# Optimization experiments

Measured on AMD Instinct MI355X. Metric: run time of the kernel, lower is better.

Reference implementation:

```python
import jax, jax.numpy as jnp
import numpy as np

SCALE = 4.0
GRID = 64
B, T, A, C = 4, 256, 3, 13
F = 5 + C  # x,y,z,r,conf,cls...


def setup_inputs() -> dict:
    key = jax.random.key(0)
    k1, k2, k3, k4, k5 = jax.random.split(key, 5)
    p = jax.random.normal(k1, (B, A, GRID, GRID, GRID, F), dtype=jnp.float32)
    xyz = jax.random.uniform(k2, (B, T, 3), minval=4.0, maxval=SCALE * GRID - 4.0)
    r = jax.random.uniform(k3, (B, T, 1), minval=6.0, maxval=20.0)
    conf = (jax.random.uniform(k4, (B, T, 1)) < 0.6).astype(jnp.float32)
    cls = jax.nn.one_hot(jax.random.randint(k5, (B, T), 0, C), C, dtype=jnp.float32)
    targets = jnp.concatenate([xyz, r, conf, cls], axis=-1)  # [B,T,18]
    anchor = jnp.array([[[8.0], [12.0], [16.0]]], dtype=jnp.float32)  # [1,A,1]
    return {"p": p, "targets": targets, "anchor": anchor}


def _bce(logits, t):
    # BCEWithLogitsLoss (pos_weight=1), elementwise
    return t * jax.nn.softplus(-logits) + (1.0 - t) * jax.nn.softplus(logits)


def _eiou(box1, box2, eps=1e-7):
    # boxes are (x,y,z,r): axis-aligned cubes of side r centered at xyz (3D EIoU)
    c1, r1 = box1[:, :3], box1[:, 3]
    c2, r2 = box2[:, :3], box2[:, 3]
    h1, h2 = r1[:, None] * 0.5, r2[:, None] * 0.5
    lo = jnp.maximum(c1 - h1, c2 - h2)
    hi = jnp.minimum(c1 + h1, c2 + h2)
    inter = jnp.prod(jnp.clip(hi - lo, 0.0), axis=-1)
    union = r1 ** 3 + r2 ** 3 - inter + eps
    iou = inter / union
    clo = jnp.minimum(c1 - h1, c2 - h2)
    chi = jnp.maximum(c1 + h1, c2 + h2)
    cdim = chi - clo  # enclosing box per-axis extent
    rho2 = jnp.sum((c1 - c2) ** 2, axis=-1)
    c2diag = jnp.sum(cdim ** 2, axis=-1) + eps
    size_pen = jnp.sum(((r1 - r2) ** 2)[:, None] / (cdim ** 2 + eps), axis=-1)
    return iou - rho2 / c2diag - size_pen


def reference(p, targets, anchor):
    Bs, An, K, J, I, Fd = p.shape
    Cn = Fd - 5
    g, gr = 0.5, 0.0
    Tn = targets.shape[1]
    n = Bs * Tn
    x = targets.reshape(n, Fd)
    b0 = jnp.repeat(jnp.arange(Bs), Tn)
    conf_m = x[:, 4] > 0.5
    anchor_norm = anchor[0] / SCALE  # [A,1]
    gxyzr = x[:, :4] / SCALE
    rn = gxyzr[:, 3]
    ratio = rn[None, :] / anchor_norm  # [A,n]
    aok = jnp.maximum(ratio, 1.0 / ratio) < 4.0
    gxyz = gxyzr[:, :3]
    gdim = jnp.array([K, J, I], dtype=p.dtype)  # gain[1:]
    gxyz_i = gdim - gxyz
    m1 = (gxyz % 1.0 < g) & (gxyz > 1.0)
    m2 = (gxyz_i % 1.0 < g) & (gxyz_i > 1.0)
    fm = jnp.stack([jnp.ones_like(m1[:, 0]), m1[:, 0], m1[:, 1], m1[:, 2], m2[:, 0], m2[:, 1], m2[:, 2]])  # [7,n]
    off = jnp.array([[0, 0, 0], [1, 0, 0], [0, 1, 0], [0, 0, 1], [-1, 0, 0], [0, -1, 0], [0, 0, -1]], dtype=p.dtype) * g
    valid = (conf_m[None, None, :] & aok[None, :, :] & fm[:, None, :]).reshape(-1)  # [7*A*n]
    bidx = jnp.broadcast_to(b0[None, None, :], (7, An, n)).reshape(-1)
    aidx = jnp.broadcast_to(jnp.arange(An)[None, :, None], (7, An, n)).reshape(-1)
    gxyz_c = jnp.broadcast_to(gxyz[None, None], (7, An, n, 3))
    off_c = jnp.broadcast_to(off[:, None, None, :], (7, An, n, 3))
    gijk_f = jnp.trunc(jax.lax.stop_gradient(gxyz_c - off_c))  # torch .long() truncates
    gijk = gijk_f.astype(jnp.int32).reshape(-1, 3)
    gi = jnp.clip(gijk[:, 0], 0, I - 1)
    gj = jnp.clip(gijk[:, 1], 0, J - 1)
    gk = jnp.clip(gijk[:, 2], 0, K - 1)
    tbox = jnp.concatenate([(gxyz_c - gijk_f).reshape(-1, 3), jnp.broadcast_to(rn[None, None, :], (7, An, n)).reshape(-1, 1)], axis=1)
    anchors = anchor_norm[aidx]  # [N,1]
    tcls = jnp.broadcast_to(x[None, None, :, 5:], (7, An, n, Cn)).reshape(-1, Cn)
    pred = p[bidx, aidx, gk, gj, gi]  # [N,F]
    pxyz = jax.nn.sigmoid(pred[:, :3]) * 2.0 - 0.5
    pr = (jax.nn.sigmoid(pred[:, 3:4]) * 2.0) ** 2 * anchors
    pbox = jnp.concatenate([pxyz, pr], axis=1)
    ei = _eiou(pbox, tbox)
    w = valid.astype(p.dtype)
    nv = jnp.maximum(jnp.sum(w), 1.0)
    loss_bbox = jnp.sum(w * (1.0 - ei)) / nv  # masked mean == torch mean over filtered rows
    iou_d = jax.lax.stop_gradient(jnp.clip(ei, 0.0))
    objv = (1.0 - gr) + gr * iou_d  # gr=0 -> 1.0
    tobj = jnp.zeros((Bs, An, K, J, I), dtype=p.dtype).at[bidx, aidx, gk, gj, gi].max(w * objv)
    loss_cls = jnp.sum(w[:, None] * _bce(pred[:, 5:], tcls)) / (nv * Cn)
    loss_obj = jnp.mean(_bce(p[..., 4], tobj))
    lb = loss_bbox * 1.0
    lo = loss_obj * 20.0
    lc = loss_cls * 10.0
    return ((lb + lo + lc) * Bs, lo, lc)
```

## Files before the change

### kernel.cpp

```cpp
#include <hip/hip_runtime.h>
#include <math.h>

#define NTGT   1024
#define NCAND  (21 * NTGT)
#define NCBLK  (NCAND / 256)
#define NCELL  (4 * 3 * 64 * 64 * 64)
#define BITW   (NCELL / 32)
#define NBLK   2048

__device__ __forceinline__ float softplusf(float x) {
    return fmaxf(x, 0.0f) + __logf(1.0f + __expf(-fabsf(x)));
}
__device__ __forceinline__ float sigmoidf(float x) {
    return 1.0f / (1.0f + __expf(-x));
}

__global__ __launch_bounds__(256) void fused_kernel(
    const float* __restrict__ p, const float* __restrict__ tg,
    const float* __restrict__ anchor, float* __restrict__ acc,
    unsigned int* __restrict__ bitmap)
{
    if (blockIdx.x < NCBLK) {
        int idx = blockIdx.x * 256 + threadIdx.x;
        float nv_v = 0.f, bb_v = 0.f, cl_v = 0.f, ob_v = 0.f;
        {
            int t  = idx & (NTGT - 1);
            int oa = idx >> 10;
            int a  = oa % 3;
            int o  = oa / 3;
            const float* x = tg + t * 18;
            float conf = x[4];
            float rn   = x[3] * 0.25f;
            float an   = anchor[a] * 0.25f;
            float ratio = rn / an;
            bool ok = (conf > 0.5f) && (fmaxf(ratio, 1.0f / ratio) < 4.0f);
            float gv[3] = { x[0] * 0.25f, x[1] * 0.25f, x[2] * 0.25f };
            float off[3] = { 0.f, 0.f, 0.f };
            if (o >= 1) {
                if (o <= 3) {
                    int c = o - 1;
                    float v = gv[c];
                    ok = ok && ((v - floorf(v)) < 0.5f) && (v > 1.0f);
                    off[c] = 0.5f;
                } else {
                    int c = o - 4;
                    float vi = 64.0f - gv[c];
                    ok = ok && ((vi - floorf(vi)) < 0.5f) && (vi > 1.0f);
                    off[c] = -0.5f;
                }
            }
            if (ok) {
                float tb[3]; int gq[3];
                #pragma unroll
                for (int c = 0; c < 3; c++) {
                    float f = truncf(gv[c] - off[c]);
                    tb[c] = gv[c] - f;
                    gq[c] = min(max((int)f, 0), 63);
                }
                int b0 = t >> 8;
                unsigned int cell =
                    ((((unsigned)(b0 * 3 + a) * 64u + (unsigned)gq[2]) * 64u
                      + (unsigned)gq[1]) * 64u) + (unsigned)gq[0];
                const float* pp = p + (size_t)cell * 18u;
                float pd[18];
                #pragma unroll
                for (int f = 0; f < 18; f++) pd[f] = pp[f];

                float c1[3];
                #pragma unroll
                for (int c = 0; c < 3; c++) c1[c] = sigmoidf(pd[c]) * 2.0f - 0.5f;
                float s4 = sigmoidf(pd[3]) * 2.0f;
                float r1 = s4 * s4 * an;
                float r2 = rn;

                float h1 = 0.5f * r1, h2 = 0.5f * r2;
                float inter = 1.f, rho2 = 0.f, c2d = 0.f, spen = 0.f;
                float dr2 = (r1 - r2) * (r1 - r2);
                #pragma unroll
                for (int c = 0; c < 3; c++) {
                    float lo1 = c1[c] - h1, hi1 = c1[c] + h1;
                    float lo2 = tb[c] - h2, hi2 = tb[c] + h2;
                    inter *= fmaxf(fminf(hi1, hi2) - fmaxf(lo1, lo2), 0.f);
                    float cd  = fmaxf(hi1, hi2) - fminf(lo1, lo2);
                    float cd2 = cd * cd;
                    float d   = c1[c] - tb[c];
                    rho2 += d * d;
                    c2d  += cd2;
                    spen += dr2 / (cd2 + 1e-7f);
                }
                float uni = r1 * r1 * r1 + r2 * r2 * r2 - inter + 1e-7f;
                float ei  = inter / uni - rho2 / (c2d + 1e-7f) - spen;

                nv_v = 1.0f;
                bb_v = 1.0f - ei;
                float cl = 0.f;
                #pragma unroll
                for (int c = 0; c < 13; c++) {
                    float l = pd[5 + c];
                    cl += softplusf(l) - x[5 + c] * l;
                }
                cl_v = cl;
                unsigned int old = atomicOr(&bitmap[cell >> 5], 1u << (cell & 31u));
                if (!(old & (1u << (cell & 31u)))) ob_v = pd[4];
            }
        }
        #pragma unroll
        for (int s = 32; s > 0; s >>= 1) {
            nv_v += __shfl_down(nv_v, s, 64);
            bb_v += __shfl_down(bb_v, s, 64);
            cl_v += __shfl_down(cl_v, s, 64);
            ob_v += __shfl_down(ob_v, s, 64);
        }
        if ((threadIdx.x & 63) == 0 && nv_v != 0.f) {
            atomicAdd(&acc[0], nv_v);
            atomicAdd(&acc[1], bb_v);
            atomicAdd(&acc[2], cl_v);
            atomicAdd(&acc[4], ob_v);
        }
    }

    float s = 0.f;
    {
        int i = blockIdx.x * 256 + threadIdx.x;
        #pragma unroll
        for (int it = 0; it < NCELL / (NBLK * 256); it++) {
            s += softplusf(p[(size_t)i * 18u + 4u]);
            i += NBLK * 256;
        }
    }
    #pragma unroll
    for (int sh = 32; sh > 0; sh >>= 1) s += __shfl_down(s, sh, 64);
    __shared__ float sm[4];
    int lane = threadIdx.x & 63, w = threadIdx.x >> 6;
    if (lane == 0) sm[w] = s;
    __syncthreads();
    if (threadIdx.x == 0) {
        atomicAdd(&acc[3], sm[0] + sm[1] + sm[2] + sm[3]);
    }
}

__global__ void final_kernel(const float* __restrict__ acc, float* __restrict__ out)
{
    float nv = fmaxf(acc[0], 1.0f);
    float lb = acc[1] / nv;
    float lc = acc[2] / (nv * 13.0f) * 10.0f;
    float lo = (acc[3] - acc[4]) * (20.0f / (float)NCELL);
    out[0] = (lb + lo + lc) * 4.0f;
    out[1] = lo;
    out[2] = lc;
}

extern "C" void kernel_launch(void* const* d_in, const int* in_sizes, int n_in,
                              void* d_out, int out_size, void* d_ws, size_t ws_size,
                              hipStream_t stream) {
    const float* p       = (const float*)d_in[0];
    const float* targets = (const float*)d_in[1];
    const float* anchor  = (const float*)d_in[2];
    float* out = (float*)d_out;

    float* acc = (float*)d_ws;
    unsigned int* bitmap = (unsigned int*)((char*)d_ws + 32);

    hipMemsetAsync(d_ws, 0, 32 + (size_t)BITW * 4, stream);

    fused_kernel<<<NBLK, 256, 0, stream>>>(p, targets, anchor, acc, bitmap);
    final_kernel<<<1, 1, 0, stream>>>(acc, out);
}
```

Baseline: 311.0 us.

## Fold final reduction into fused kernel via last-block counter

Removes the separate single-thread finalize launch. The last block to finish, detected with an atomic counter behind a threadfence, computes the three loss outputs itself. It also adds a min-blocks launch bound of 8 and reads prediction fields directly from global memory instead of staging all 18 into registers, aiming to cut register pressure and raise occupancy. The main risks are the atomic counter's ordering and possible repeated loads from pp.

```diff
diff --git a/kernel.cpp b/kernel.cpp
--- a/kernel.cpp
+++ b/kernel.cpp
@@ -7,6 +7,7 @@
 #define NCELL  (4 * 3 * 64 * 64 * 64)
 #define BITW   (NCELL / 32)
 #define NBLK   2048
+#define SITER  (NCELL / (NBLK * 256))
 
 __device__ __forceinline__ float softplusf(float x) {
     return fmaxf(x, 0.0f) + __logf(1.0f + __expf(-fabsf(x)));
@@ -15,10 +16,11 @@
     return 1.0f / (1.0f + __expf(-x));
 }
 
-__global__ __launch_bounds__(256) void fused_kernel(
+__global__ __launch_bounds__(256, 8) void fused_kernel(
     const float* __restrict__ p, const float* __restrict__ tg,
     const float* __restrict__ anchor, float* __restrict__ acc,
-    unsigned int* __restrict__ bitmap)
+    unsigned int* __restrict__ ctr, unsigned int* __restrict__ bitmap,
+    float* __restrict__ out)
 {
     if (blockIdx.x < NCBLK) {
         int idx = blockIdx.x * 256 + threadIdx.x;
@@ -62,14 +64,12 @@
                     ((((unsigned)(b0 * 3 + a) * 64u + (unsigned)gq[2]) * 64u
                       + (unsigned)gq[1]) * 64u) + (unsigned)gq[0];
                 const float* pp = p + (size_t)cell * 18u;
-                float pd[18];
-                #pragma unroll
-                for (int f = 0; f < 18; f++) pd[f] = pp[f];
 
                 float c1[3];
                 #pragma unroll
-                for (int c = 0; c < 3; c++) c1[c] = sigmoidf(pd[c]) * 2.0f - 0.5f;
-                float s4 = sigmoidf(pd[3]) * 2.0f;
+                for (int c = 0; c < 3; c++) c1[c] = sigmoidf(pp[c]) * 2.0f - 0.5f;
+                float s4 = sigmoidf(pp[3]) * 2.0f;
+                float p4 = pp[4];
                 float r1 = s4 * s4 * an;
                 float r2 = rn;
 
@@ -96,12 +96,12 @@
                 float cl = 0.f;
                 #pragma unroll
                 for (int c = 0; c < 13; c++) {
-                    float l = pd[5 + c];
+                    float l = pp[5 + c];
                     cl += softplusf(l) - x[5 + c] * l;
                 }
                 cl_v = cl;
                 unsigned int old = atomicOr(&bitmap[cell >> 5], 1u << (cell & 31u));
-                if (!(old & (1u << (cell & 31u)))) ob_v = pd[4];
+                if (!(old & (1u << (cell & 31u)))) ob_v = p4;
             }
         }
         #pragma unroll
@@ -121,11 +121,10 @@
 
     float s = 0.f;
     {
-        int i = blockIdx.x * 256 + threadIdx.x;
+        size_t base = (size_t)(blockIdx.x * 256 + threadIdx.x);
         #pragma unroll
-        for (int it = 0; it < NCELL / (NBLK * 256); it++) {
-            s += softplusf(p[(size_t)i * 18u + 4u]);
-            i += NBLK * 256;
+        for (int it = 0; it < SITER; it++) {
+            s += softplusf(p[(base + (size_t)it * (NBLK * 256)) * 18u + 4u]);
         }
     }
     #pragma unroll
@@ -137,17 +136,27 @@
     if (threadIdx.x == 0) {
         atomicAdd(&acc[3], sm[0] + sm[1] + sm[2] + sm[3]);
     }
-}
 
-__global__ void final_kernel(const float* __restrict__ acc, float* __restrict__ out)
-{
-    float nv = fmaxf(acc[0], 1.0f);
-    float lb = acc[1] / nv;
-    float lc = acc[2] / (nv * 13.0f) * 10.0f;
-    float lo = (acc[3] - acc[4]) * (20.0f / (float)NCELL);
-    out[0] = (lb + lo + lc) * 4.0f;
-    out[1] = lo;
-    out[2] = lc;
+    __shared__ bool last;
+    if (threadIdx.x == 0) {
+        __threadfence();
+        unsigned int prev = atomicAdd(ctr, 1u);
+        last = (prev == NBLK - 1);
+    }
+    __syncthreads();
+    if (last && threadIdx.x == 0) {
+        float nv = fmaxf(atomicAdd(&acc[0], 0.f), 1.0f);
+        float bb = atomicAdd(&acc[1], 0.f);
+        float cl = atomicAdd(&acc[2], 0.f);
+        float sp = atomicAdd(&acc[3], 0.f);
+        float cp = atomicAdd(&acc[4], 0.f);
+        float lb = bb / nv;
+        float lc = cl / (nv * 13.0f) * 10.0f;
+        float lo = (sp - cp) * (20.0f / (float)NCELL);
+        out[0] = (lb + lo + lc) * 4.0f;
+        out[1] = lo;
+        out[2] = lc;
+    }
 }
 
 extern "C" void kernel_launch(void* const* d_in, const int* in_sizes, int n_in,
@@ -159,10 +168,11 @@
     float* out = (float*)d_out;
 
     float* acc = (float*)d_ws;
+    unsigned int* ctr    = (unsigned int*)((char*)d_ws + 24);
     unsigned int* bitmap = (unsigned int*)((char*)d_ws + 32);
 
     hipMemsetAsync(d_ws, 0, 32 + (size_t)BITW * 4, stream);
 
-    fused_kernel<<<NBLK, 256, 0, stream>>>(p, targets, anchor, acc, bitmap);
-    final_kernel<<<1, 1, 0, stream>>>(acc, out);
+    fused_kernel<<<NBLK, 256, 0, stream>>>(p, targets, anchor, acc, ctr,
+                                           bitmap, out);
 }
```

Result: slower. 412.3 us (+32.6%).
